# Kernel tuning notes

Measured on AMD Instinct MI355X. Metric: run time of the kernel, lower is better.

Reference implementation:

```python
import jax, jax.numpy as jnp
import numpy as np

M = 16    # manifold dim = latent_dim // 2
HID = 64  # metric MLP hidden width


def metric_single(x, W1, b1, W2, b2):
    """Metric tensor for a single point x: (m,) -> SPD (m, m)."""
    h = jnp.tanh(x @ W1 + b1)
    A = (h @ W2 + b2).reshape(M, M)
    return A @ A.T + jnp.eye(M, dtype=x.dtype)


def connection_coeffs(x, W1, b1, W2, b2):
    """Christoffel symbols Gamma^k_ab, shape (B, m, m, m)."""
    f = lambda xs: metric_single(xs, W1, b1, W2, b2)
    # partial_g[B, a, i, b] = d g_{ai} / d x_b
    partial_g = jax.vmap(jax.jacfwd(f))(x)
    g = jax.vmap(f)(x)                      # (B, m, m)
    inv_g = jnp.linalg.inv(g)               # small 16x16 inverses
    t1 = jnp.einsum('Bki,Baib->Bkab', inv_g, partial_g)
    t2 = jnp.einsum('Bki,Bbai->Bkab', inv_g, partial_g)
    t3 = jnp.einsum('Bki,Biab->Bkab', inv_g, partial_g)
    return 0.5 * (t1 + t2 - t3)


def geodesic_ode_f(z, W1, b1, W2, b2):
    """RHS of geodesic ODE; z = [x, v] of shape (B, 2m)."""
    x = z[:, :M]
    v = z[:, M:]
    Gamma = connection_coeffs(x, W1, b1, W2, b2)
    dv = -jnp.einsum('Bkab,Ba,Bb->Bk', Gamma, v, v)
    return jnp.concatenate([v, dv], axis=1)


def rk4_step(z, dt, f):
    k1 = f(z)
    k2 = f(z + 0.5 * dt * k1)
    k3 = f(z + 0.5 * dt * k2)
    k4 = f(z + dt * k3)
    return z + dt / 6.0 * (k1 + 2 * k2 + 2 * k3 + k4)


def setup_inputs() -> dict:
    key = jax.random.key(0)
    ks = jax.random.split(key, 5)
    B = 16384
    z = jax.random.normal(ks[0], (B, 2 * M), dtype=jnp.float32) * 0.5
    t = jnp.asarray(1.0, dtype=jnp.float32)
    W1 = jax.random.normal(ks[1], (M, HID), dtype=jnp.float32) * 0.3
    b1 = jax.random.normal(ks[2], (HID,), dtype=jnp.float32) * 0.1
    W2 = jax.random.normal(ks[3], (HID, M * M), dtype=jnp.float32) * 0.05
    b2 = jax.random.normal(ks[4], (M * M,), dtype=jnp.float32) * 0.05
    return {"z": z, "t": t, "W1": W1, "b1": b1, "W2": W2, "b2": b2, "num_steps": 4}


def reference(z, t, W1, b1, W2, b2, num_steps):
    """Geodesic exponential map exp(x0, v0, t) via num_steps RK4 steps."""
    dt = t / num_steps
    f = lambda zz: geodesic_ode_f(zz, W1, b1, W2, b2)
    for _ in range(num_steps):  # small fixed sequential loop (num_steps=4)
        z = rk4_step(z, dt, f)
    return z
```

## Files before the change

### kernel.cpp

```cpp
#include <hip/hip_runtime.h>
#include <math.h>


typedef _Float16 f16;
typedef _Float16 f16x2 __attribute__((ext_vector_type(2)));
typedef _Float16 f16x4 __attribute__((ext_vector_type(4)));
typedef _Float16 f16x8 __attribute__((ext_vector_type(8)));
typedef __fp16 h16x2 __attribute__((ext_vector_type(2)));
typedef float f32x2 __attribute__((ext_vector_type(2)));
typedef float f32x4 __attribute__((ext_vector_type(4)));
typedef float f32x16 __attribute__((ext_vector_type(16)));

#define SAG_P 392
#define SZ_P  36
#define SH_P  72
#define SW_P  20
#define SWP_C 20

__device__ __forceinline__ float fastTanh(float x) {
    float e = exp2f(x * 2.885390081777927f);
    return 1.0f - 2.0f * __builtin_amdgcn_rcpf(1.0f + e);
}

__device__ __forceinline__ f16x2 pk2(float a, float b) {
    h16x2 p = __builtin_amdgcn_cvt_pkrtz(a, b);
    return __builtin_bit_cast(f16x2, p);
}

typedef union { f16x4 v4; f16x2 v2[2]; } u16x4;
typedef union { f16x8 v8; f16x2 v2[4]; int i32[4]; } u16x8;

template<int K>
__device__ __forceinline__ float bcf(float x) {
    int v = __builtin_amdgcn_mov_dpp(__builtin_bit_cast(int, x),
                                     0x150 | K, 0xf, 0xf, false);
    return __builtin_bit_cast(float, v);
}

template<int K>
__device__ __forceinline__ void fe_all2(float (&R0)[17], float (&R1)[17],
                                        const int i16, float &inv0, float &inv1) {
    if constexpr (K < 16) {
        float p0 = bcf<K>(R0[K]);
        float p1 = bcf<K>(R1[K]);
        float pi0 = __builtin_amdgcn_rcpf(p0);
        float pi1 = __builtin_amdgcn_rcpf(p1);
        if (i16 == K) { inv0 = pi0; inv1 = pi1; }
        float f0 = (i16 == K) ? 0.0f : R0[K] * pi0;
        float f1 = (i16 == K) ? 0.0f : R1[K] * pi1;
        #pragma unroll
        for (int j = K + 1; j <= 16; ++j) {
            float v0 = bcf<K>(R0[j]);
            float v1 = bcf<K>(R1[j]);
            R0[j] -= f0 * v0;
            R1[j] -= f1 * v1;
        }
        fe_all2<K + 1>(R0, R1, i16, inv0, inv1);
    }
}

__global__ __launch_bounds__(256, 1)
void geo_kernel(const float* __restrict__ zin, const float* __restrict__ tg,
                const float* __restrict__ W1g, const float* __restrict__ b1g,
                const float* __restrict__ W2g, const float* __restrict__ b2g,
                const int* __restrict__ nsg, float* __restrict__ outg, int B)
{
    __shared__ __align__(16) f16   sAG[2][16 * SAG_P];
    __shared__ __align__(16) f16   sHT[2][16 * SH_P];
    __shared__ __align__(16) float sZI[2][16 * SZ_P];
    __shared__ __align__(16) float sKV[2][16 * SW_P];
    __shared__ __align__(16) float sWp[2][4 * 16 * SWP_C];

    const int tid = threadIdx.x;
    const int w = tid >> 6;
    const int l = tid & 63;
    const int i16 = l & 15, q4 = l >> 4, h2 = l >> 5, sc = q4 & 1;

    f16x8 w2a[4][2];
    #pragma unroll
    for (int t = 0; t < 4; ++t)
        #pragma unroll
        for (int ch = 0; ch < 2; ++ch)
            #pragma unroll
            for (int j = 0; j < 8; ++j)
                w2a[t][ch][j] = (f16)W2g[(8*q4 + j + 32*ch)*256 + i16 + 16*(4*w + t)];

    f16x8 w2r[8];
    #pragma unroll
    for (int ch = 0; ch < 8; ++ch)
        #pragma unroll
        for (int j = 0; j < 8; ++j)
            w2r[ch][j] = (f16)W2g[(i16 + 16*w)*256 + 8*q4 + j + 32*ch];

    f16x8 w1h;
    #pragma unroll
    for (int j = 0; j < 8; ++j) {
        int k = 8*q4 + j;
        w1h[j] = (k < 16) ? (f16)W1g[k*64 + i16 + 16*w] : (f16)0.0f;
    }

    f16x8 w1q[2];
    #pragma unroll
    for (int ch = 0; ch < 2; ++ch)
        #pragma unroll
        for (int j = 0; j < 8; ++j)
            w1q[ch][j] = (f16)W1g[i16*64 + 8*q4 + j + 32*ch];

    float b2v[4][4];
    #pragma unroll
    for (int t = 0; t < 4; ++t)
        #pragma unroll
        for (int reg = 0; reg < 4; ++reg)
            b2v[t][reg] = b2g[16*(4*w + t) + 4*q4 + reg];
    float b1v[4];
    #pragma unroll
    for (int reg = 0; reg < 4; ++reg) b1v[reg] = b1g[16*w + 4*q4 + reg];

    const int pb = blockIdx.x * 32;
    const int p_cmb = tid >> 4;
    const int g16 = tid & 15;
    f32x2 zc[2], ar[2];
    #pragma unroll
    for (int g = 0; g < 2; ++g) {
        int pl = pb + 16*g + p_cmb;
        int pg = (pl < B) ? pl : (B - 1);
        zc[g] = *(const f32x2*)&zin[pg*32 + 2*g16];
        *(f32x2*)&sZI[g][p_cmb*SZ_P + 2*g16] = zc[g];
    }
    __syncthreads();

    const float tv = tg[0];
    const int nst = nsg[0];
    const float dt = tv / (float)nst;

    const int xmask = (q4 >= 2) ? 0 : -1;

    #pragma unroll 1
    for (int st = 0; st < nst; ++st) {
        #pragma unroll 1
        for (int s = 0; s < 4; ++s) {
            float dreg[2][4];
            #pragma unroll
            for (int g = 0; g < 2; ++g) {
                u16x8 xf;
                {
                    f32x4 xa = *(const f32x4*)&sZI[g][i16*SZ_P + 8*sc];
                    f32x4 xb = *(const f32x4*)&sZI[g][i16*SZ_P + 8*sc + 4];
                    xf.v2[0] = pk2(xa[0], xa[1]);
                    xf.v2[1] = pk2(xa[2], xa[3]);
                    xf.v2[2] = pk2(xb[0], xb[1]);
                    xf.v2[3] = pk2(xb[2], xb[3]);
                    #pragma unroll
                    for (int jp = 0; jp < 4; ++jp) xf.i32[jp] &= xmask;
                }
                f32x4 hc = {0.f, 0.f, 0.f, 0.f};
                hc = __builtin_amdgcn_mfma_f32_16x16x32_f16(w1h, xf.v8, hc, 0, 0, 0);
                float hv[4];
                #pragma unroll
                for (int reg = 0; reg < 4; ++reg) {
                    hv[reg] = fastTanh(hc[reg] + b1v[reg]);
                    dreg[g][reg] = hv[reg]*hv[reg] - 1.0f;
                }
                u16x4 hv4;
                hv4.v2[0] = pk2(hv[0], hv[1]);
                hv4.v2[1] = pk2(hv[2], hv[3]);
                *(f16x4*)&sHT[g][i16*SH_P + 16*w + 4*q4] = hv4.v4;
            }
            __syncthreads();
            #pragma unroll
            for (int g = 0; g < 2; ++g) {
                f32x4 vA = *(const f32x4*)&sZI[g][i16*SZ_P + 16 + 4*w];
                f16x8 hf0 = *(const f16x8*)&sHT[g][i16*SH_P + 8*q4];
                f16x8 hf1 = *(const f16x8*)&sHT[g][i16*SH_P + 8*q4 + 32];
                float pw[4] = {0.f, 0.f, 0.f, 0.f};
                #pragma unroll
                for (int t = 0; t < 4; ++t) {
                    f32x4 ac = {0.f, 0.f, 0.f, 0.f};
                    ac = __builtin_amdgcn_mfma_f32_16x16x32_f16(w2a[t][0], hf0, ac, 0, 0, 0);
                    ac = __builtin_amdgcn_mfma_f32_16x16x32_f16(w2a[t][1], hf1, ac, 0, 0, 0);
                    float a0 = ac[0] + b2v[t][0], a1 = ac[1] + b2v[t][1];
                    float a2 = ac[2] + b2v[t][2], a3 = ac[3] + b2v[t][3];
                    float vv = vA[t];
                    pw[0] += vv * a0; pw[1] += vv * a1;
                    pw[2] += vv * a2; pw[3] += vv * a3;
                    u16x4 av;
                    av.v2[0] = pk2(a0, a1);
                    av.v2[1] = pk2(a2, a3);
                    *(f16x4*)&sAG[g][i16*SAG_P + 24*(4*w + t) + 4*q4] = av.v4;
                }
                f32x4 pwv = {pw[0], pw[1], pw[2], pw[3]};
                *(f32x4*)&sWp[g][(w*16 + i16)*SWP_C + 4*q4] = pwv;
            }
            __syncthreads();
            #pragma unroll
            for (int g = 0; g < 2; ++g) {
                #pragma unroll
                for (int u0 = 0; u0 < 2; ++u0) {
                    int u = 2*w + u0;
                    int pt = 2*u + sc;
                    f16x8 af = *(const f16x8*)&sAG[g][pt*SAG_P + 24*i16 + 8*h2];
                    f32x16 gz = {0.0f};
                    f32x16 gacc = __builtin_amdgcn_mfma_f32_32x32x16_f16(af, af, gz, 0, 0, 0);
                    float gv[8];
                    #pragma unroll
                    for (int rr = 0; rr < 4; ++rr) {
                        float lo0 = gacc[rr],     hi0 = gacc[rr + 8];
                        float lo1 = gacc[rr + 4], hi1 = gacc[rr + 12];
                        float g0 = sc ? hi0 : lo0;
                        float g1 = sc ? hi1 : lo1;
                        int a0 = 4*h2 + rr;
                        int a1 = 8 + 4*h2 + rr;
                        gv[rr]     = g0 + ((i16 == a0) ? 1.0f : 0.0f);
                        gv[4 + rr] = g1 + ((i16 == a1) ? 1.0f : 0.0f);
                    }
                    u16x4 g0p, g1p;
                    g0p.v2[0] = pk2(gv[0], gv[1]); g0p.v2[1] = pk2(gv[2], gv[3]);
                    g1p.v2[0] = pk2(gv[4], gv[5]); g1p.v2[1] = pk2(gv[6], gv[7]);
                    *(f16x4*)&sAG[g][pt*SAG_P + 24*i16 + 4*h2]     = g0p.v4;
                    *(f16x4*)&sAG[g][pt*SAG_P + 24*i16 + 8 + 4*h2] = g1p.v4;
                }
            }
            #pragma unroll
            for (int g = 0; g < 2; ++g) {
                float vch[8];
                {
                    const float* vp = &sZI[g][i16*SZ_P + 16 + (q4 >> 1)];
                    #pragma unroll
                    for (int c = 0; c < 8; ++c) vch[c] = vp[2*c];
                }
                float wv[8];
                {
                    f32x4 s0 = *(const f32x4*)&sWp[g][(0*16 + i16)*SWP_C + 8*sc];
                    f32x4 s1 = *(const f32x4*)&sWp[g][(1*16 + i16)*SWP_C + 8*sc];
                    f32x4 s2 = *(const f32x4*)&sWp[g][(2*16 + i16)*SWP_C + 8*sc];
                    f32x4 s3 = *(const f32x4*)&sWp[g][(3*16 + i16)*SWP_C + 8*sc];
                    f32x4 t0 = *(const f32x4*)&sWp[g][(0*16 + i16)*SWP_C + 8*sc + 4];
                    f32x4 t1 = *(const f32x4*)&sWp[g][(1*16 + i16)*SWP_C + 8*sc + 4];
                    f32x4 t2 = *(const f32x4*)&sWp[g][(2*16 + i16)*SWP_C + 8*sc + 4];
                    f32x4 t3 = *(const f32x4*)&sWp[g][(3*16 + i16)*SWP_C + 8*sc + 4];
                    #pragma unroll
                    for (int j = 0; j < 4; ++j) {
                        wv[j]     = s0[j] + s1[j] + s2[j] + s3[j];
                        wv[4 + j] = t0[j] + t1[j] + t2[j] + t3[j];
                    }
                }
                f16x2 wfp[4];
                #pragma unroll
                for (int jp = 0; jp < 4; ++jp) wfp[jp] = pk2(wv[2*jp], wv[2*jp + 1]);
                f32x4 racc = {0.f, 0.f, 0.f, 0.f};
                #pragma unroll
                for (int ch = 0; ch < 8; ++ch) {
                    f16 vvh = (f16)vch[ch];
                    f16x2 vv2; vv2.x = vvh; vv2.y = vvh;
                    u16x8 uf;
                    #pragma unroll
                    for (int jp = 0; jp < 4; ++jp) uf.v2[jp] = vv2 * wfp[jp];
                    racc = __builtin_amdgcn_mfma_f32_16x16x32_f16(w2r[ch], uf.v8, racc, 0, 0, 0);
                }
                u16x4 tv4;
                tv4.v2[0] = pk2(dreg[g][0]*racc[0], dreg[g][1]*racc[1]);
                tv4.v2[1] = pk2(dreg[g][2]*racc[2], dreg[g][3]*racc[3]);
                *(f16x4*)&sHT[g][i16*SH_P + 16*w + 4*q4] = tv4.v4;
            }
            __syncthreads();
            #pragma unroll
            for (int g = 0; g < 2; ++g) {
                int ptq = 4*w + (i16 & 3);
                f16x8 tb0 = *(const f16x8*)&sHT[g][ptq*SH_P + 8*q4];
                f16x8 tb1 = *(const f16x8*)&sHT[g][ptq*SH_P + 8*q4 + 32];
                f32x4 qa = {0.f, 0.f, 0.f, 0.f};
                qa = __builtin_amdgcn_mfma_f32_16x16x32_f16(w1q[0], tb0, qa, 0, 0, 0);
                qa = __builtin_amdgcn_mfma_f32_16x16x32_f16(w1q[1], tb1, qa, 0, 0, 0);
                if (i16 < 4) {
                    #pragma unroll
                    for (int reg = 0; reg < 4; ++reg)
                        sAG[g][(4*w + i16)*SAG_P + 24*(4*q4 + reg) + 16] = (f16)qa[reg];
                }
            }
            {
                __builtin_amdgcn_s_setprio(1);
                const int psl = 4*w + q4;
                float R0[17], R1[17];
                {
                    const f16* rp0 = &sAG[0][psl*SAG_P + 24*i16];
                    const f16* rp1 = &sAG[1][psl*SAG_P + 24*i16];
                    f16x8 ra0 = *(const f16x8*)&rp0[0];
                    f16x8 rb0 = *(const f16x8*)&rp0[8];
                    f16x8 ra1 = *(const f16x8*)&rp1[0];
                    f16x8 rb1 = *(const f16x8*)&rp1[8];
                    #pragma unroll
                    for (int j = 0; j < 8; ++j) {
                        R0[j] = (float)ra0[j]; R0[8+j] = (float)rb0[j];
                        R1[j] = (float)ra1[j]; R1[8+j] = (float)rb1[j];
                    }
                    R0[16] = (float)rp0[16];
                    R1[16] = (float)rp1[16];
                }
                float inv0 = 1.0f, inv1 = 1.0f;
                fe_all2<0>(R0, R1, i16, inv0, inv1);
                sKV[0][psl*SW_P + i16] = R0[16] * inv0;
                sKV[1][psl*SW_P + i16] = R1[16] * inv1;
                __builtin_amdgcn_s_setprio(0);
            }
            #pragma unroll
            for (int g = 0; g < 2; ++g) {
                f32x2 kk;
                if (g16 < 8) kk = *(const f32x2*)&sZI[g][p_cmb*SZ_P + 16 + 2*g16];
                else         kk = *(const f32x2*)&sKV[g][p_cmb*SW_P + 2*(g16 - 8)];
                if (s == 0) ar[g] = kk;
                else {
                    float wgt = (s == 3) ? 1.0f : 2.0f;
                    ar[g].x += wgt * kk.x; ar[g].y += wgt * kk.y;
                }
                f32x2 zi;
                if (s < 3) {
                    float alpha = (s < 2) ? (0.5f * dt) : dt;
                    zi.x = zc[g].x + alpha * kk.x; zi.y = zc[g].y + alpha * kk.y;
                } else {
                    float c6 = dt / 6.0f;
                    zc[g].x += c6 * ar[g].x; zc[g].y += c6 * ar[g].y;
                    zi = zc[g];
                }
                *(f32x2*)&sZI[g][p_cmb*SZ_P + 2*g16] = zi;
            }
            __syncthreads();
        }
    }
    #pragma unroll
    for (int g = 0; g < 2; ++g) {
        int pl = pb + 16*g + p_cmb;
        if (pl < B)
            *(f32x2*)&outg[pl*32 + 2*g16] = zc[g];
    }
}

extern "C" void kernel_launch(void* const* d_in, const int* in_sizes, int n_in,
                              void* d_out, int out_size, void* d_ws, size_t ws_size,
                              hipStream_t stream) {
    (void)n_in; (void)d_ws; (void)ws_size; (void)out_size;
    const float* z  = (const float*)d_in[0];
    const float* t  = (const float*)d_in[1];
    const float* W1 = (const float*)d_in[2];
    const float* b1 = (const float*)d_in[3];
    const float* W2 = (const float*)d_in[4];
    const float* b2 = (const float*)d_in[5];
    const int*   ns = (const int*)d_in[6];
    float* out = (float*)d_out;
    const int B = in_sizes[0] / 32;
    int grid = (B + 31) / 32;
    hipLaunchKernelGGL(geo_kernel, dim3(grid), dim3(256), 0, stream,
                       z, t, W1, b1, W2, b2, ns, out, B);
}
```

Before: 162.1 us.

## Factor metric before RHS is ready and interleave elimination with MFMA chain

Splits the per-point Gauss-Jordan solve into two parts. The elimination of the 16x16 metric now runs first, recording its multipliers, and it is interleaved round by round with the MFMA accumulation that builds the right-hand side, so VALU/DPP work overlaps matrix-core latency. After the barrier only a cheap 16-step chain is applied to the augmented column. The cost is more live registers (two multiplier arrays of 16 plus both accumulators), which may raise register pressure.

```diff
diff --git a/kernel.cpp b/kernel.cpp
--- a/kernel.cpp
+++ b/kernel.cpp
@@ -38,24 +38,68 @@
 }
 
 template<int K>
-__device__ __forceinline__ void fe_all2(float (&R0)[17], float (&R1)[17],
+__device__ __forceinline__ void roundGF(float (&R0)[16], float (&R1)[16],
+                                        float (&f0)[16], float (&f1)[16],
                                         const int i16, float &inv0, float &inv1) {
+    float p0 = bcf<K>(R0[K]);
+    float p1 = bcf<K>(R1[K]);
+    float pi0 = __builtin_amdgcn_rcpf(p0);
+    float pi1 = __builtin_amdgcn_rcpf(p1);
+    if (i16 == K) { inv0 = pi0; inv1 = pi1; }
+    float a = (i16 == K) ? 0.0f : R0[K] * pi0;
+    float b = (i16 == K) ? 0.0f : R1[K] * pi1;
+    f0[K] = a; f1[K] = b;
+    #pragma unroll
+    for (int j = K + 1; j < 16; ++j) {
+        float v0 = bcf<K>(R0[j]);
+        float v1 = bcf<K>(R1[j]);
+        R0[j] -= a * v0;
+        R1[j] -= b * v1;
+    }
+}
+
+template<int CH>
+__device__ __forceinline__ void rsolveCh(const f16x8 (&w2rA)[8],
+    const float (&vch0)[8], const float (&vch1)[8],
+    const f16x2 (&wfp0)[4], const f16x2 (&wfp1)[4],
+    f32x4 &racc0, f32x4 &racc1,
+    float (&R0)[16], float (&R1)[16],
+    float (&f0)[16], float (&f1)[16],
+    const int i16, float &inv0, float &inv1)
+{
+    if constexpr (CH < 8) {
+        {
+            f16 vvh = (f16)vch0[CH];
+            f16x2 vv2; vv2.x = vvh; vv2.y = vvh;
+            u16x8 uf;
+            #pragma unroll
+            for (int jp = 0; jp < 4; ++jp) uf.v2[jp] = vv2 * wfp0[jp];
+            racc0 = __builtin_amdgcn_mfma_f32_16x16x32_f16(w2rA[CH], uf.v8, racc0, 0, 0, 0);
+        }
+        roundGF<2*CH>(R0, R1, f0, f1, i16, inv0, inv1);
+        {
+            f16 vvh = (f16)vch1[CH];
+            f16x2 vv2; vv2.x = vvh; vv2.y = vvh;
+            u16x8 uf;
+            #pragma unroll
+            for (int jp = 0; jp < 4; ++jp) uf.v2[jp] = vv2 * wfp1[jp];
+            racc1 = __builtin_amdgcn_mfma_f32_16x16x32_f16(w2rA[CH], uf.v8, racc1, 0, 0, 0);
+        }
+        roundGF<2*CH+1>(R0, R1, f0, f1, i16, inv0, inv1);
+        rsolveCh<CH+1>(w2rA, vch0, vch1, wfp0, wfp1, racc0, racc1,
+                       R0, R1, f0, f1, i16, inv0, inv1);
+    }
+}
+
+template<int K>
+__device__ __forceinline__ void augchain(float &a0, float &a1,
+                                         const float (&f0)[16], const float (&f1)[16]) {
     if constexpr (K < 16) {
-        float p0 = bcf<K>(R0[K]);
-        float p1 = bcf<K>(R1[K]);
-        float pi0 = __builtin_amdgcn_rcpf(p0);
-        float pi1 = __builtin_amdgcn_rcpf(p1);
-        if (i16 == K) { inv0 = pi0; inv1 = pi1; }
-        float f0 = (i16 == K) ? 0.0f : R0[K] * pi0;
-        float f1 = (i16 == K) ? 0.0f : R1[K] * pi1;
-        #pragma unroll
-        for (int j = K + 1; j <= 16; ++j) {
-            float v0 = bcf<K>(R0[j]);
-            float v1 = bcf<K>(R1[j]);
-            R0[j] -= f0 * v0;
-            R1[j] -= f1 * v1;
-        }
-        fe_all2<K + 1>(R0, R1, i16, inv0, inv1);
+        float b0 = bcf<K>(a0);
+        float b1 = bcf<K>(a1);
+        a0 -= f0[K] * b0;
+        a1 -= f1[K] * b1;
+        augchain<K + 1>(a0, a1, f0, f1);
     }
 }
 
@@ -220,14 +264,14 @@
                     *(f16x4*)&sAG[g][pt*SAG_P + 24*i16 + 8 + 4*h2] = g1p.v4;
                 }
             }
-            #pragma unroll
-            for (int g = 0; g < 2; ++g) {
-                float vch[8];
-                {
-                    const float* vp = &sZI[g][i16*SZ_P + 16 + (q4 >> 1)];
-                    #pragma unroll
-                    for (int c = 0; c < 8; ++c) vch[c] = vp[2*c];
-                }
+            const int psl = 4*w + q4;
+            float vchA[2][8];
+            f16x2 wfpA[2][4];
+            #pragma unroll
+            for (int g = 0; g < 2; ++g) {
+                const float* vp = &sZI[g][i16*SZ_P + 16 + (q4 >> 1)];
+                #pragma unroll
+                for (int c = 0; c < 8; ++c) vchA[g][c] = vp[2*c];
                 float wv[8];
                 {
                     f32x4 s0 = *(const f32x4*)&sWp[g][(0*16 + i16)*SWP_C + 8*sc];
@@ -244,23 +288,39 @@
                         wv[4 + j] = t0[j] + t1[j] + t2[j] + t3[j];
                     }
                 }
-                f16x2 wfp[4];
-                #pragma unroll
-                for (int jp = 0; jp < 4; ++jp) wfp[jp] = pk2(wv[2*jp], wv[2*jp + 1]);
-                f32x4 racc = {0.f, 0.f, 0.f, 0.f};
-                #pragma unroll
-                for (int ch = 0; ch < 8; ++ch) {
-                    f16 vvh = (f16)vch[ch];
-                    f16x2 vv2; vv2.x = vvh; vv2.y = vvh;
-                    u16x8 uf;
-                    #pragma unroll
-                    for (int jp = 0; jp < 4; ++jp) uf.v2[jp] = vv2 * wfp[jp];
-                    racc = __builtin_amdgcn_mfma_f32_16x16x32_f16(w2r[ch], uf.v8, racc, 0, 0, 0);
-                }
+                #pragma unroll
+                for (int jp = 0; jp < 4; ++jp) wfpA[g][jp] = pk2(wv[2*jp], wv[2*jp + 1]);
+            }
+            float RG0[16], RG1[16];
+            {
+                const f16* rp0 = &sAG[0][psl*SAG_P + 24*i16];
+                const f16* rp1 = &sAG[1][psl*SAG_P + 24*i16];
+                f16x8 ra0 = *(const f16x8*)&rp0[0];
+                f16x8 rb0 = *(const f16x8*)&rp0[8];
+                f16x8 ra1 = *(const f16x8*)&rp1[0];
+                f16x8 rb1 = *(const f16x8*)&rp1[8];
+                #pragma unroll
+                for (int j = 0; j < 8; ++j) {
+                    RG0[j] = (float)ra0[j]; RG0[8+j] = (float)rb0[j];
+                    RG1[j] = (float)ra1[j]; RG1[8+j] = (float)rb1[j];
+                }
+            }
+            f32x4 racc0 = {0.f, 0.f, 0.f, 0.f};
+            f32x4 racc1 = {0.f, 0.f, 0.f, 0.f};
+            float fA0[16], fA1[16];
+            float inv0 = 1.0f, inv1 = 1.0f;
+            __builtin_amdgcn_s_setprio(1);
+            rsolveCh<0>(w2r, vchA[0], vchA[1], wfpA[0], wfpA[1],
+                        racc0, racc1, RG0, RG1, fA0, fA1, i16, inv0, inv1);
+            __builtin_amdgcn_s_setprio(0);
+            {
                 u16x4 tv4;
-                tv4.v2[0] = pk2(dreg[g][0]*racc[0], dreg[g][1]*racc[1]);
-                tv4.v2[1] = pk2(dreg[g][2]*racc[2], dreg[g][3]*racc[3]);
-                *(f16x4*)&sHT[g][i16*SH_P + 16*w + 4*q4] = tv4.v4;
+                tv4.v2[0] = pk2(dreg[0][0]*racc0[0], dreg[0][1]*racc0[1]);
+                tv4.v2[1] = pk2(dreg[0][2]*racc0[2], dreg[0][3]*racc0[3]);
+                *(f16x4*)&sHT[0][i16*SH_P + 16*w + 4*q4] = tv4.v4;
+                tv4.v2[0] = pk2(dreg[1][0]*racc1[0], dreg[1][1]*racc1[1]);
+                tv4.v2[1] = pk2(dreg[1][2]*racc1[2], dreg[1][3]*racc1[3]);
+                *(f16x4*)&sHT[1][i16*SH_P + 16*w + 4*q4] = tv4.v4;
             }
             __syncthreads();
             #pragma unroll
@@ -278,28 +338,12 @@
                 }
             }
             {
+                float a0 = (float)sAG[0][psl*SAG_P + 24*i16 + 16];
+                float a1 = (float)sAG[1][psl*SAG_P + 24*i16 + 16];
                 __builtin_amdgcn_s_setprio(1);
-                const int psl = 4*w + q4;
-                float R0[17], R1[17];
-                {
-                    const f16* rp0 = &sAG[0][psl*SAG_P + 24*i16];
-                    const f16* rp1 = &sAG[1][psl*SAG_P + 24*i16];
-                    f16x8 ra0 = *(const f16x8*)&rp0[0];
-                    f16x8 rb0 = *(const f16x8*)&rp0[8];
-                    f16x8 ra1 = *(const f16x8*)&rp1[0];
-                    f16x8 rb1 = *(const f16x8*)&rp1[8];
-                    #pragma unroll
-                    for (int j = 0; j < 8; ++j) {
-                        R0[j] = (float)ra0[j]; R0[8+j] = (float)rb0[j];
-                        R1[j] = (float)ra1[j]; R1[8+j] = (float)rb1[j];
-                    }
-                    R0[16] = (float)rp0[16];
-                    R1[16] = (float)rp1[16];
-                }
-                float inv0 = 1.0f, inv1 = 1.0f;
-                fe_all2<0>(R0, R1, i16, inv0, inv1);
-                sKV[0][psl*SW_P + i16] = R0[16] * inv0;
-                sKV[1][psl*SW_P + i16] = R1[16] * inv1;
+                augchain<0>(a0, a1, fA0, fA1);
+                sKV[0][psl*SW_P + i16] = a0 * inv0;
+                sKV[1][psl*SW_P + i16] = a1 * inv1;
                 __builtin_amdgcn_s_setprio(0);
             }
             #pragma unroll
```

Result: no change. 160.8 us (-0.8%).
